# Kernel optimization log

Measured on AMD Instinct MI355X. Metric: run time of the kernel, lower is better.

Reference implementation:

```python
import jax, jax.numpy as jnp
import numpy as np

N = 2048; E = 65536; T = 6; F_IN = 2
H_ENC = 256; LAT = 128; H_DEC = 256
PRED = 6
MIN_X, MAX_X = 0.0, 1.0
MIN_Y, MAX_Y = 0.0, 1.0
MIN_EW, MAX_EW = 0.0, 0.5
VISUAL_RANGE = 0.5


def setup_inputs() -> dict:
    key = jax.random.key(0)
    ks = jax.random.split(key, 17)
    p = lambda k, shape: jax.random.normal(k, shape, jnp.float32) * 0.05
    return {
        "x_seq": jax.random.uniform(ks[0], (T, N, F_IN), jnp.float32),
        "edge_index_seq": jax.random.randint(ks[1], (T, 2, E), 0, N),
        "edge_weight_seq": jax.random.uniform(ks[2], (T, E), jnp.float32, 1e-3, 1.0),
        "h_enc": jnp.zeros((N, H_ENC), jnp.float32),
        "h_dec": jnp.zeros((N, H_DEC), jnp.float32),
        "enc_Wx": p(ks[3], (3, 2, F_IN, H_ENC)),
        "enc_bx": p(ks[4], (3, H_ENC)),
        "enc_Wh": p(ks[5], (3, 2, H_ENC, H_ENC)),
        "enc_bh": p(ks[6], (3, H_ENC)),
        "enc_lin_W": p(ks[7], (H_ENC, LAT)),
        "enc_lin_b": p(ks[8], (LAT,)),
        "dec_Wx": p(ks[9], (3, 2, LAT, H_DEC)),
        "dec_bx": p(ks[10], (3, H_DEC)),
        "dec_Wh": p(ks[11], (3, 2, H_DEC, H_DEC)),
        "dec_bh": p(ks[12], (3, H_DEC)),
        "dec_lin_W": p(ks[13], (H_DEC, F_IN)),
        "dec_lin_b": p(ks[14], (F_IN,)),
    }


def _sparse_conv_fn(edge_index, edge_weight, n):
    # ChebConv K=2, sym normalization, lambda_max=2 => T1(L_hat) = -D^-1/2 A D^-1/2
    src, dst = edge_index[0], edge_index[1]
    deg = jax.ops.segment_sum(edge_weight, src, num_segments=n)
    dinv = jnp.where(deg > 0, jax.lax.rsqrt(jnp.where(deg > 0, deg, 1.0)), 0.0)
    norm = -dinv[src] * edge_weight * dinv[dst]  # [E]

    def conv(x, W, b):  # W: [2, in, out]
        tx1 = jax.ops.segment_sum(norm[:, None] * x[src], dst, num_segments=n)
        return x @ W[0] + tx1 @ W[1] + b
    return conv


def _dense_conv_fn(y_hat):
    # graph rebuilt from detached predicted coords (radius graph, dense masked form)
    c = jax.lax.stop_gradient(y_hat)
    px = c[:, 0] * (MAX_X - MIN_X) + MIN_X
    py = c[:, 1] * (MAX_Y - MIN_Y) + MIN_Y
    coords = jnp.stack((px, py), axis=1)  # [N, 2]
    d = jnp.linalg.norm(coords[:, None, :] - coords[None, :, :], axis=2)  # [N, N]
    mask = (d < VISUAL_RANGE) & (d > 0)
    w = jnp.where(mask, (d - MIN_EW) / (MAX_EW - MIN_EW), 0.0)
    deg = w.sum(axis=1)
    dinv = jnp.where(deg > 0, jax.lax.rsqrt(jnp.where(deg > 0, deg, 1.0)), 0.0)
    M = -(dinv[:, None] * w) * dinv[None, :]  # scaled-Laplacian off-diagonal

    def conv(x, W, b):
        return x @ W[0] + (M @ x) @ W[1] + b
    return conv


def _gru(conv, x, H, Wx, bx, Wh, bh):
    # GConvGRU gates: each gate = conv_x(X) + conv_h(H)
    z = jax.nn.sigmoid(conv(x, Wx[0], bx[0]) + conv(H, Wh[0], bh[0]))
    r = jax.nn.sigmoid(conv(x, Wx[1], bx[1]) + conv(H, Wh[1], bh[1]))
    h_tilde = jnp.tanh(conv(x, Wx[2], bx[2]) + conv(H * r, Wh[2], bh[2]))
    return z * H + (1.0 - z) * h_tilde


def reference(x_seq, edge_index_seq, edge_weight_seq, h_enc, h_dec,
              enc_Wx, enc_bx, enc_Wh, enc_bh, enc_lin_W, enc_lin_b,
              dec_Wx, dec_bx, dec_Wh, dec_bh, dec_lin_W, dec_lin_b):
    n = x_seq.shape[1]

    def step(conv, x, he, hd):
        he0 = _gru(conv, x, he, enc_Wx, enc_bx, enc_Wh, enc_bh)
        z = jax.nn.relu(he0) @ enc_lin_W + enc_lin_b
        hd0 = _gru(conv, z, hd, dec_Wx, dec_bx, dec_Wh, dec_bh)
        y_hat = jax.nn.relu(hd0) @ dec_lin_W + dec_lin_b
        return y_hat, he0, hd0

    # observed snapshots (sparse edge-list graphs)
    for t in range(x_seq.shape[0]):
        conv = _sparse_conv_fn(edge_index_seq[t], edge_weight_seq[t], n)
        y_hat, h_enc, h_dec = step(conv, x_seq[t], h_enc, h_dec)

    preds = [y_hat]
    for _ in range(PRED - 1):
        conv = _dense_conv_fn(y_hat)
        y_hat, h_enc, h_dec = step(conv, y_hat, h_enc, h_dec)
        preds.append(y_hat)
    return jnp.stack(preds)  # [PRED, N, 2]
```

## Files before the change

### kernel.cpp

```cpp
#include <hip/hip_runtime.h>
#include <math.h>

#define NN 2048
#define EE 65536
#define T_OBS 6
#define FIN 2
#define HE 256
#define LT 128
#define XC 384
#define PREDN 6
#define DMM_NZ 8
#define ZR_NZ 4
#define GT_NZ 8
#define LIN_NZ 8

typedef __attribute__((ext_vector_type(8))) short short8v;
typedef __attribute__((ext_vector_type(4))) short short4v;
typedef __attribute__((ext_vector_type(4))) float float4v;

static __device__ __forceinline__ unsigned short f2bf(float f) {
    union { float f; unsigned u; } v; v.f = f;
    unsigned r = v.u + 0x7fff + ((v.u >> 16) & 1);
    return (unsigned short)(r >> 16);
}

static __device__ __forceinline__ void bfsplit(float f, unsigned short& h,
                                               unsigned short& l) {
    unsigned u = __float_as_uint(f);
    h = (unsigned short)(u >> 16);
    float hf = __uint_as_float(u & 0xffff0000u);
    l = (unsigned short)(__float_as_uint(f - hf) >> 16);
}

static __device__ __forceinline__ float bf2f(unsigned short b) {
    return __uint_as_float(((unsigned)b) << 16);
}

__global__ void k_degcnt_lds(const int* __restrict__ ei, const float* __restrict__ ews,
                             float* __restrict__ deg_all, int* __restrict__ cnt_all) {
    __shared__ float ldeg[NN];
    __shared__ int lcnt[NN];
    int tg = blockIdx.y;
    const int* src = ei + (size_t)tg * 2 * EE;
    const int* dst = src + EE;
    const float* ew = ews + (size_t)tg * EE;
    for (int i = threadIdx.x; i < NN; i += 256) { ldeg[i] = 0.f; lcnt[i] = 0; }
    __syncthreads();
    const int EPB = EE / 8;
    int e0 = blockIdx.x * EPB;
    for (int e = e0 + threadIdx.x; e < e0 + EPB; e += 256) {
        atomicAdd(&ldeg[src[e]], ew[e]);
        atomicAdd(&lcnt[dst[e]], 1);
    }
    __syncthreads();
    for (int i = threadIdx.x; i < NN; i += 256) {
        float d = ldeg[i]; int cc = lcnt[i];
        if (d != 0.f) atomicAdd(&deg_all[tg * NN + i], d);
        if (cc) atomicAdd(&cnt_all[tg * NN + i], cc);
    }
}

__global__ void k_scan_b(const int* __restrict__ cnt_all, const float* __restrict__ deg_all,
                         int* __restrict__ roff_all, int* __restrict__ cur_all,
                         float* __restrict__ dinv_all) {
    __shared__ int part[256];
    int tg = blockIdx.x;
    const int* cnt = cnt_all + tg * NN;
    const float* deg = deg_all + tg * NN;
    int* roff = roff_all + tg * (NN + 1);
    int* cur = cur_all + tg * NN;
    float* dinv = dinv_all + tg * NN;
    int t = threadIdx.x;
#pragma unroll
    for (int i = t; i < NN; i += 256) {
        float d = deg[i];
        dinv[i] = d > 0.f ? 1.f / sqrtf(d) : 0.f;
    }
    int loc[8];
    int s = 0;
#pragma unroll
    for (int i = 0; i < 8; i++) { loc[i] = cnt[t * 8 + i]; s += loc[i]; }
    part[t] = s;
    __syncthreads();
    for (int off = 1; off < 256; off <<= 1) {
        int v = (t >= off) ? part[t - off] : 0;
        __syncthreads();
        part[t] += v;
        __syncthreads();
    }
    int run = (t == 0) ? 0 : part[t - 1];
#pragma unroll
    for (int i = 0; i < 8; i++) {
        int idx = t * 8 + i;
        roff[idx] = run;
        cur[idx] = run;
        run += loc[i];
    }
    if (t == 255) roff[NN] = run;
}

__global__ void k_scatter2_b(const int* __restrict__ ei, const float* __restrict__ ews,
                             const float* __restrict__ dinv_all, int* __restrict__ cur_all,
                             int* __restrict__ csr_src_all, float* __restrict__ csr_nrm_all) {
    int tg = blockIdx.y;
    int e = blockIdx.x * blockDim.x + threadIdx.x;
    const int* src = ei + (size_t)tg * 2 * EE;
    const int* dst = src + EE;
    const float* ew = ews + (size_t)tg * EE;
    const float* dinv = dinv_all + tg * NN;
    if (e < EE) {
        int s = src[e], d = dst[e];
        int p = atomicAdd(&cur_all[tg * NN + d], 1);
        csr_src_all[(size_t)tg * EE + p] = s;
        csr_nrm_all[(size_t)tg * EE + p] = -dinv[s] * ew[e] * dinv[d];
    }
}

__global__ void k_spmm2_b(const int* __restrict__ roff_all, const int* __restrict__ csr_src_all,
                          const float* __restrict__ csr_nrm_all, const float* __restrict__ x_seq,
                          float* __restrict__ aggx_all) {
    int tg = blockIdx.y;
    int nid = blockIdx.x * blockDim.x + threadIdx.x;
    if (nid < NN) {
        const int* roff = roff_all + tg * (NN + 1);
        const int* csr_src = csr_src_all + (size_t)tg * EE;
        const float* csr_nrm = csr_nrm_all + (size_t)tg * EE;
        const float* X = x_seq + (size_t)tg * NN * FIN;
        int s0 = roff[nid], s1 = roff[nid + 1];
        float a0 = 0.f, a1 = 0.f;
        for (int s = s0; s < s1; ++s) {
            int i = csr_src[s]; float w = csr_nrm[s];
            float2 xv = *(const float2*)&X[2 * i];
            a0 = fmaf(w, xv.x, a0);
            a1 = fmaf(w, xv.y, a1);
        }
        aggx_all[(size_t)tg * NN * FIN + 2 * nid] = a0;
        aggx_all[(size_t)tg * NN * FIN + 2 * nid + 1] = a1;
    }
}

template <int F, int TPN>
__global__ void k_spmm_vb(const int* __restrict__ roff, const int* __restrict__ csr_src,
                          const float* __restrict__ csr_nrm,
                          const unsigned short* __restrict__ Xb,
                          float* __restrict__ out, int ldo) {
    const int NPB = 256 / TPN;
    int w = threadIdx.x / TPN, l = threadIdx.x % TPN;
    int nid = blockIdx.x * NPB + w;
    int c = l << 2;
    int s0 = roff[nid], s1 = roff[nid + 1];
    float4 acc = make_float4(0.f, 0.f, 0.f, 0.f);
    int s = s0;
    for (; s + 8 <= s1; s += 8) {
        int is[8]; float ws[8];
#pragma unroll
        for (int j = 0; j < 8; j++) { is[j] = csr_src[s + j]; ws[j] = csr_nrm[s + j]; }
        if (c < F) {
            short4v xv[8];
#pragma unroll
            for (int j = 0; j < 8; j++)
                xv[j] = *(const short4v*)&Xb[(size_t)is[j] * F + c];
#pragma unroll
            for (int j = 0; j < 8; j++) {
                acc.x = fmaf(ws[j], bf2f((unsigned short)xv[j][0]), acc.x);
                acc.y = fmaf(ws[j], bf2f((unsigned short)xv[j][1]), acc.y);
                acc.z = fmaf(ws[j], bf2f((unsigned short)xv[j][2]), acc.z);
                acc.w = fmaf(ws[j], bf2f((unsigned short)xv[j][3]), acc.w);
            }
        }
    }
    for (; s < s1; ++s) {
        int i0 = csr_src[s]; float w0 = csr_nrm[s];
        if (c < F) {
            short4v xv = *(const short4v*)&Xb[(size_t)i0 * F + c];
            acc.x = fmaf(w0, bf2f((unsigned short)xv[0]), acc.x);
            acc.y = fmaf(w0, bf2f((unsigned short)xv[1]), acc.y);
            acc.z = fmaf(w0, bf2f((unsigned short)xv[2]), acc.z);
            acc.w = fmaf(w0, bf2f((unsigned short)xv[3]), acc.w);
        }
    }
    if (c < F) *(float4*)&out[(size_t)nid * ldo + c] = acc;
}

__global__ void k_ddeg(const float* __restrict__ c, float* __restrict__ dinv) {
    int i = blockIdx.x;
    int t = threadIdx.x;
    float xi = c[2 * i], yi = c[2 * i + 1];
    float s = 0.f;
    for (int j = t; j < NN; j += 256) {
        float dx = xi - c[2 * j], dy = yi - c[2 * j + 1];
        float d = sqrtf(dx * dx + dy * dy);
        if (d > 0.f && d < 0.5f) s += 2.f * d;
    }
    __shared__ float red[256];
    red[t] = s;
    __syncthreads();
    for (int off = 128; off > 0; off >>= 1) {
        if (t < off) red[t] += red[t + off];
        __syncthreads();
    }
    if (t == 0) {
        float d = red[0];
        dinv[i] = d > 0.f ? 1.f / sqrtf(d) : 0.f;
    }
}

__global__ void k_dM2(const float* __restrict__ c, const float* __restrict__ dinv,
                      unsigned short* __restrict__ Mb, float* __restrict__ ax) {
    int i = blockIdx.x;
    int t = threadIdx.x;
    float xi = c[2 * i], yi = c[2 * i + 1], di = dinv[i];
    float a0 = 0.f, a1 = 0.f;
    for (int j = t; j < NN; j += 256) {
        float dx = xi - c[2 * j], dy = yi - c[2 * j + 1];
        float d = sqrtf(dx * dx + dy * dy);
        float w = (d > 0.f && d < 0.5f) ? 2.f * d : 0.f;
        float v = -(di * w) * dinv[j];
        Mb[(size_t)i * NN + j] = f2bf(v);
        a0 = fmaf(v, c[2 * j], a0);
        a1 = fmaf(v, c[2 * j + 1], a1);
    }
    __shared__ float r0[256], r1[256];
    r0[t] = a0;
    r1[t] = a1;
    __syncthreads();
    for (int off = 128; off > 0; off >>= 1) {
        if (t < off) { r0[t] += r0[t + off]; r1[t] += r1[t + off]; }
        __syncthreads();
    }
    if (t == 0) { ax[2 * i] = r0[0]; ax[2 * i + 1] = r1[0]; }
}

template <int F>
__global__ __launch_bounds__(256) void k_dmm_mfb(
    const unsigned short* __restrict__ Mb, const unsigned short* __restrict__ Xb,
    float* __restrict__ pbuf)
{
    __shared__ __align__(16) unsigned short Ms[64][72];
    __shared__ __align__(16) unsigned short Xs[64][72];
    const int tid = threadIdx.x;
    const int wid = tid >> 6, lane = tid & 63;
    const int m0 = blockIdx.x << 6, n0 = blockIdx.y << 6;
    const int kb0 = blockIdx.z << 8;
    const int lr = lane & 15;
    const int kg = lane >> 4;
    float4v acc[4];
#pragma unroll
    for (int t = 0; t < 4; t++) acc[t] = (float4v){0.f, 0.f, 0.f, 0.f};

    for (int kb = kb0; kb < kb0 + 256; kb += 64) {
#pragma unroll
        for (int it = 0; it < 2; it++) {
            int i = tid + it * 256;
            int r = i >> 3, c8 = (i & 7) << 3;
            *(short8v*)&Ms[r][c8] =
                *(const short8v*)&Mb[(size_t)(m0 + r) * NN + kb + c8];
        }
#pragma unroll
        for (int it = 0; it < 2; it++) {
            int i = tid + it * 256;
            int k2 = (i & 31) << 1;
            int n4 = (i >> 5) << 2;
            short4v va = *(const short4v*)&Xb[(size_t)(kb + k2) * F + n0 + n4];
            short4v vb = *(const short4v*)&Xb[(size_t)(kb + k2 + 1) * F + n0 + n4];
#pragma unroll
            for (int j = 0; j < 4; j++)
                *(unsigned*)&Xs[n4 + j][k2] =
                    (unsigned)(unsigned short)va[j] |
                    ((unsigned)(unsigned short)vb[j] << 16);
        }
        __syncthreads();
#pragma unroll
        for (int kh = 0; kh < 2; kh++) {
            int kk = kh * 32 + kg * 8;
            short8v a = *(const short8v*)&Ms[(wid << 4) + lr][kk];
#pragma unroll
            for (int t = 0; t < 4; t++) {
                short8v b = *(const short8v*)&Xs[(t << 4) + lr][kk];
                acc[t] = __builtin_amdgcn_mfma_f32_16x16x32_bf16(a, b, acc[t], 0, 0, 0);
            }
        }
        __syncthreads();
    }
    float* p = pbuf + (size_t)blockIdx.z * NN * F;
#pragma unroll
    for (int t = 0; t < 4; t++)
#pragma unroll
        for (int j = 0; j < 4; j++)
            p[(size_t)(m0 + (wid << 4) + (kg << 2) + j) * F + n0 + (t << 4) + lr] =
                acc[t][j];
}

template <int F, int NZ>
__global__ void k_redks(const float* __restrict__ pbuf, float* __restrict__ out) {
    const int TOT = NN * F / 4;
    int i = blockIdx.x * blockDim.x + threadIdx.x;
    if (i < TOT) {
        const float4* p = (const float4*)pbuf;
        float4 s = p[i];
#pragma unroll
        for (int z = 1; z < NZ; z++) {
            float4 v = p[(size_t)z * TOT + i];
            s.x += v.x; s.y += v.y; s.z += v.z; s.w += v.w;
        }
        ((float4*)out)[i] = s;
    }
}

template <bool RELU>
__device__ __forceinline__ void mfma_seg(
    unsigned short (*Ah)[40], unsigned short (*Al)[40],
    unsigned short (*Bh)[40], unsigned short (*Bl)[40],
    const float* __restrict__ A, int lda,
    const float* __restrict__ B, int ldb, int K,
    int m0, int tid, int wid, int lr, int kg, float4v (&acc)[4])
{
    for (int k0 = 0; k0 < K; k0 += 32) {
        {
            int r = tid >> 2, k8 = (tid & 3) << 3;
            const float* ap = &A[(size_t)(m0 + r) * lda + k0 + k8];
            float4 va = *(const float4*)ap;
            float4 vb = *(const float4*)(ap + 4);
            float v[8] = {va.x, va.y, va.z, va.w, vb.x, vb.y, vb.z, vb.w};
            short8v hv, lv;
#pragma unroll
            for (int j = 0; j < 8; j++) {
                float f = RELU ? fmaxf(v[j], 0.f) : v[j];
                unsigned short h, l;
                bfsplit(f, h, l);
                hv[j] = (short)h; lv[j] = (short)l;
            }
            *(short8v*)&Ah[r][k8] = hv;
            *(short8v*)&Al[r][k8] = lv;
        }
        {
            int k2 = (tid & 15) << 1;
            int n4 = (tid >> 4) << 2;
            const float* bp = &B[(size_t)(k0 + k2) * ldb + n4];
            float4 va = *(const float4*)bp;
            float4 vb = *(const float4*)(bp + ldb);
            float v0[4] = {va.x, va.y, va.z, va.w};
            float v1[4] = {vb.x, vb.y, vb.z, vb.w};
#pragma unroll
            for (int j = 0; j < 4; j++) {
                unsigned short h0, l0, h1, l1;
                bfsplit(v0[j], h0, l0);
                bfsplit(v1[j], h1, l1);
                *(unsigned*)&Bh[n4 + j][k2] = (unsigned)h0 | ((unsigned)h1 << 16);
                *(unsigned*)&Bl[n4 + j][k2] = (unsigned)l0 | ((unsigned)l1 << 16);
            }
        }
        __syncthreads();
        short8v ah = *(short8v*)&Ah[(wid << 4) + lr][kg << 3];
        short8v al = *(short8v*)&Al[(wid << 4) + lr][kg << 3];
#pragma unroll
        for (int t = 0; t < 4; t++) {
            short8v bh = *(short8v*)&Bh[(t << 4) + lr][kg << 3];
            short8v bl = *(short8v*)&Bl[(t << 4) + lr][kg << 3];
            acc[t] = __builtin_amdgcn_mfma_f32_16x16x32_bf16(ah, bh, acc[t], 0, 0, 0);
            acc[t] = __builtin_amdgcn_mfma_f32_16x16x32_bf16(ah, bl, acc[t], 0, 0, 0);
            acc[t] = __builtin_amdgcn_mfma_f32_16x16x32_bf16(al, bh, acc[t], 0, 0, 0);
        }
        __syncthreads();
    }
}

__global__ __launch_bounds__(256) void k_zr_ks(
    const float* __restrict__ A0, int K01, const float* __restrict__ A1,
    const float* __restrict__ H, const float* __restrict__ A3,
    int la1, int la2, int la3,
    const float* __restrict__ Wx, const float* __restrict__ Wh,
    float* __restrict__ pbuf)
{
    __shared__ __align__(16) unsigned short Ah[64][40], Al[64][40],
                                            Bh[64][40], Bl[64][40];
    int tid = threadIdx.x;
    int wid = tid >> 6, lane = tid & 63, lr = lane & 15, kg = lane >> 4;
    int m0 = blockIdx.x << 6;
    int g = blockIdx.y >> 2;
    int n0 = (blockIdx.y & 3) << 6;
    float4v acc[4];
#pragma unroll
    for (int t = 0; t < 4; t++) acc[t] = (float4v){0.f, 0.f, 0.f, 0.f};
    const float* As[4] = {A0, A1, H, A3};
    const int ldas[4] = {K01, la1, la2, la3};
    const float* Bs[4] = {
        Wx + (size_t)(g * 2 + 0) * K01 * HE + n0,
        Wx + (size_t)(g * 2 + 1) * K01 * HE + n0,
        Wh + (size_t)(g * 2 + 0) * HE * HE + n0,
        Wh + (size_t)(g * 2 + 1) * HE * HE + n0};
    const int Ks[4] = {K01, K01, HE, HE};
    int chunk = (2 * K01 + 2 * HE) / ZR_NZ;
    int lo = blockIdx.z * chunk, hi = lo + chunk;
    int off = 0;
#pragma unroll
    for (int s = 0; s < 4; s++) {
        int a = lo - off; a = a < 0 ? 0 : a;
        int b = hi - off; b = b > Ks[s] ? Ks[s] : b;
        if (b > a)
            mfma_seg<false>(Ah, Al, Bh, Bl, As[s] + a, ldas[s],
                            Bs[s] + (size_t)a * HE, HE, b - a,
                            m0, tid, wid, lr, kg, acc);
        off += Ks[s];
    }
    float* p = pbuf + (size_t)blockIdx.z * NN * 512;
    int cbase = (g << 8) + n0;
#pragma unroll
    for (int t = 0; t < 4; t++)
#pragma unroll
        for (int j = 0; j < 4; j++)
            p[(size_t)(m0 + (wid << 4) + (kg << 2) + j) * 512 + cbase + (t << 4) + lr] =
                acc[t][j];
}

__global__ void k_zr_ep(const float* __restrict__ pbuf,
                        const float* __restrict__ bx, const float* __restrict__ bh,
                        const float* __restrict__ H,
                        const float* __restrict__ x2, const float* __restrict__ ax2,
                        const float* __restrict__ Wx,
                        float* __restrict__ gz, float* __restrict__ hr,
                        unsigned short* __restrict__ hrb)
{
    int i = blockIdx.x * 256 + threadIdx.x;
    const float4* p = (const float4*)pbuf;
    const size_t S = (size_t)NN * 512 / 4;
    float4 a = p[i];
#pragma unroll
    for (int z = 1; z < ZR_NZ; z++) {
        float4 v = p[(size_t)z * S + i];
        a.x += v.x; a.y += v.y; a.z += v.z; a.w += v.w;
    }
    int row = i >> 7, c = (i & 127) << 2;
    int g = c >> 8, cc = c & 255;
    if (Wx) {
        float x0 = x2[2 * row], x1 = x2[2 * row + 1];
        float q0 = ax2[2 * row], q1 = ax2[2 * row + 1];
        const float* W0 = Wx + (size_t)(g * 2 + 0) * FIN * HE;
        const float* W1 = Wx + (size_t)(g * 2 + 1) * FIN * HE;
        float4 w00 = *(const float4*)&W0[cc];
        float4 w01 = *(const float4*)&W0[HE + cc];
        float4 w10 = *(const float4*)&W1[cc];
        float4 w11 = *(const float4*)&W1[HE + cc];
        a.x += x0 * w00.x + x1 * w01.x + q0 * w10.x + q1 * w11.x;
        a.y += x0 * w00.y + x1 * w01.y + q0 * w10.y + q1 * w11.y;
        a.z += x0 * w00.z + x1 * w01.z + q0 * w10.z + q1 * w11.z;
        a.w += x0 * w00.w + x1 * w01.w + q0 * w10.w + q1 * w11.w;
    }
    float4 b0 = *(const float4*)&bx[c];
    float4 b1 = *(const float4*)&bh[c];
    float4 s;
    s.x = 1.f / (1.f + expf(-(a.x + b0.x + b1.x)));
    s.y = 1.f / (1.f + expf(-(a.y + b0.y + b1.y)));
    s.z = 1.f / (1.f + expf(-(a.z + b0.z + b1.z)));
    s.w = 1.f / (1.f + expf(-(a.w + b0.w + b1.w)));
    if (c < HE) {
        *(float4*)&gz[(size_t)row * HE + c] = s;
    } else {
        size_t idx = (size_t)row * HE + cc;
        float4 h = *(const float4*)&H[idx];
        s.x *= h.x; s.y *= h.y; s.z *= h.z; s.w *= h.w;
        *(float4*)&hr[idx] = s;
        short4v sb;
        sb[0] = (short)f2bf(s.x); sb[1] = (short)f2bf(s.y);
        sb[2] = (short)f2bf(s.z); sb[3] = (short)f2bf(s.w);
        *(short4v*)&hrb[idx] = sb;
    }
}

__global__ __launch_bounds__(256) void k_gt_ks(
    const float* __restrict__ A0, int K01, const float* __restrict__ A1,
    const float* __restrict__ hr, const float* __restrict__ A3,
    int la1, int la2, int la3,
    const float* __restrict__ Wx2, const float* __restrict__ Wh2,
    float* __restrict__ pbuf)
{
    __shared__ __align__(16) unsigned short Ah[64][40], Al[64][40],
                                            Bh[64][40], Bl[64][40];
    int tid = threadIdx.x;
    int wid = tid >> 6, lane = tid & 63, lr = lane & 15, kg = lane >> 4;
    int m0 = blockIdx.x << 6;
    int n0 = blockIdx.y << 6;
    float4v acc[4];
#pragma unroll
    for (int t = 0; t < 4; t++) acc[t] = (float4v){0.f, 0.f, 0.f, 0.f};
    const float* As[4] = {A0, A1, hr, A3};
    const int ldas[4] = {K01, la1, la2, la3};
    const float* Bs[4] = {
        Wx2 + n0,
        Wx2 + (size_t)K01 * HE + n0,
        Wh2 + n0,
        Wh2 + (size_t)HE * HE + n0};
    const int Ks[4] = {K01, K01, HE, HE};
    int chunk = (2 * K01 + 2 * HE) / GT_NZ;
    int lo = blockIdx.z * chunk, hi = lo + chunk;
    int off = 0;
#pragma unroll
    for (int s = 0; s < 4; s++) {
        int a = lo - off; a = a < 0 ? 0 : a;
        int b = hi - off; b = b > Ks[s] ? Ks[s] : b;
        if (b > a)
            mfma_seg<false>(Ah, Al, Bh, Bl, As[s] + a, ldas[s],
                            Bs[s] + (size_t)a * HE, HE, b - a,
                            m0, tid, wid, lr, kg, acc);
        off += Ks[s];
    }
    float* p = pbuf + (size_t)blockIdx.z * NN * HE;
#pragma unroll
    for (int t = 0; t < 4; t++)
#pragma unroll
        for (int j = 0; j < 4; j++)
            p[(size_t)(m0 + (wid << 4) + (kg << 2) + j) * HE + n0 + (t << 4) + lr] =
                acc[t][j];
}

__global__ void k_gt_ep(const float* __restrict__ pbuf,
                        const float* __restrict__ bx2, const float* __restrict__ bh2,
                        const float* __restrict__ gz,
                        const float* __restrict__ x2, const float* __restrict__ ax2,
                        const float* __restrict__ Wx2,
                        float* __restrict__ H,
                        unsigned short* __restrict__ Hb, int ldhb,
                        const float* __restrict__ dlinW, const float* __restrict__ dlinb,
                        float* __restrict__ yhat)
{
    int i = blockIdx.x * 256 + threadIdx.x;
    const float4* p = (const float4*)pbuf;
    const size_t S = (size_t)NN * HE / 4;
    float4 a = p[i];
#pragma unroll
    for (int z = 1; z < GT_NZ; z++) {
        float4 v = p[(size_t)z * S + i];
        a.x += v.x; a.y += v.y; a.z += v.z; a.w += v.w;
    }
    int row = i >> 6, c = (i & 63) << 2;
    if (Wx2) {
        float x0 = x2[2 * row], x1 = x2[2 * row + 1];
        float q0 = ax2[2 * row], q1 = ax2[2 * row + 1];
        float4 w00 = *(const float4*)&Wx2[c];
        float4 w01 = *(const float4*)&Wx2[HE + c];
        float4 w10 = *(const float4*)&Wx2[2 * HE + c];
        float4 w11 = *(const float4*)&Wx2[3 * HE + c];
        a.x += x0 * w00.x + x1 * w01.x + q0 * w10.x + q1 * w11.x;
        a.y += x0 * w00.y + x1 * w01.y + q0 * w10.y + q1 * w11.y;
        a.z += x0 * w00.z + x1 * w01.z + q0 * w10.z + q1 * w11.z;
        a.w += x0 * w00.w + x1 * w01.w + q0 * w10.w + q1 * w11.w;
    }
    float4 b0 = *(const float4*)&bx2[c];
    float4 b1 = *(const float4*)&bh2[c];
    size_t idx = (size_t)row * HE + c;
    float4 z = *(const float4*)&gz[idx];
    float4 h = *(const float4*)&H[idx];
    float4 o;
    o.x = z.x * h.x + (1.f - z.x) * tanhf(a.x + b0.x + b1.x);
    o.y = z.y * h.y + (1.f - z.y) * tanhf(a.y + b0.y + b1.y);
    o.z = z.z * h.z + (1.f - z.z) * tanhf(a.z + b0.z + b1.z);
    o.w = z.w * h.w + (1.f - z.w) * tanhf(a.w + b0.w + b1.w);
    *(float4*)&H[idx] = o;
    short4v sb;
    sb[0] = (short)f2bf(o.x); sb[1] = (short)f2bf(o.y);
    sb[2] = (short)f2bf(o.z); sb[3] = (short)f2bf(o.w);
    *(short4v*)&Hb[(size_t)row * ldhb + c] = sb;
    if (dlinW) {
        float a0 = 0.f, a1 = 0.f;
        float ov[4] = {o.x, o.y, o.z, o.w};
#pragma unroll
        for (int j = 0; j < 4; j++) {
            float v = fmaxf(ov[j], 0.f);
            float2 b = *(const float2*)&dlinW[(c + j) * 2];
            a0 = fmaf(v, b.x, a0);
            a1 = fmaf(v, b.y, a1);
        }
        for (int off = 32; off > 0; off >>= 1) {
            a0 += __shfl_down(a0, off, 64);
            a1 += __shfl_down(a1, off, 64);
        }
        if ((threadIdx.x & 63) == 0) {
            yhat[2 * row] = a0 + dlinb[0];
            yhat[2 * row + 1] = a1 + dlinb[1];
        }
    }
}

__global__ __launch_bounds__(256) void k_lin_ks(
    const float* __restrict__ A, const float* __restrict__ B,
    float* __restrict__ pbuf)
{
    __shared__ __align__(16) unsigned short Ah[64][40], Al[64][40],
                                            Bh[64][40], Bl[64][40];
    int tid = threadIdx.x;
    int wid = tid >> 6, lane = tid & 63, lr = lane & 15, kg = lane >> 4;
    int m0 = blockIdx.x << 6;
    int n0 = blockIdx.y << 6;
    int lo = blockIdx.z << 5;
    float4v acc[4];
#pragma unroll
    for (int t = 0; t < 4; t++) acc[t] = (float4v){0.f, 0.f, 0.f, 0.f};
    mfma_seg<true>(Ah, Al, Bh, Bl, A + lo, HE, B + (size_t)lo * LT + n0, LT, 32,
                   m0, tid, wid, lr, kg, acc);
    float* p = pbuf + (size_t)blockIdx.z * NN * LT;
#pragma unroll
    for (int t = 0; t < 4; t++)
#pragma unroll
        for (int j = 0; j < 4; j++)
            p[(size_t)(m0 + (wid << 4) + (kg << 2) + j) * LT + n0 + (t << 4) + lr] =
                acc[t][j];
}

__global__ void k_lin_ep(const float* __restrict__ pbuf,
                         const float* __restrict__ bias, float* __restrict__ out,
                         unsigned short* __restrict__ zb)
{
    int i = blockIdx.x * 256 + threadIdx.x;
    const float4* p = (const float4*)pbuf;
    const size_t S = (size_t)NN * LT / 4;
    int row = i >> 5, c = (i & 31) << 2;
    float4 bb = *(const float4*)&bias[c];
    float4 s = make_float4(bb.x, bb.y, bb.z, bb.w);
#pragma unroll
    for (int z = 0; z < LIN_NZ; z++) {
        float4 v = p[z * S + i];
        s.x += v.x; s.y += v.y; s.z += v.z; s.w += v.w;
    }
    ((float4*)out)[i] = s;
    short4v sb;
    sb[0] = (short)f2bf(s.x); sb[1] = (short)f2bf(s.y);
    sb[2] = (short)f2bf(s.z); sb[3] = (short)f2bf(s.w);
    *(short4v*)&zb[(size_t)row * XC + c] = sb;
}

__global__ void k_cvtb(const float* __restrict__ in, unsigned short* __restrict__ outb,
                       int ldo) {
    int i = blockIdx.x * 256 + threadIdx.x;
    int r = i >> 8, c = i & 255;
    outb[(size_t)r * ldo + c] = f2bf(in[i]);
}

extern "C" void kernel_launch(void* const* d_in, const int* in_sizes, int n_in,
                              void* d_out, int out_size, void* d_ws, size_t ws_size,
                              hipStream_t stream) {
    (void)in_sizes; (void)n_in; (void)out_size; (void)ws_size;
    const float* x_seq = (const float*)d_in[0];
    const int* ei = (const int*)d_in[1];
    const float* ews = (const float*)d_in[2];
    const float* h_enc_in = (const float*)d_in[3];
    const float* h_dec_in = (const float*)d_in[4];
    const float* encWx = (const float*)d_in[5];
    const float* encbx = (const float*)d_in[6];
    const float* encWh = (const float*)d_in[7];
    const float* encbh = (const float*)d_in[8];
    const float* elinW = (const float*)d_in[9];
    const float* elinb = (const float*)d_in[10];
    const float* decWx = (const float*)d_in[11];
    const float* decbx = (const float*)d_in[12];
    const float* decWh = (const float*)d_in[13];
    const float* decbh = (const float*)d_in[14];
    const float* dlinW = (const float*)d_in[15];
    const float* dlinb = (const float*)d_in[16];
    float* out = (float*)d_out;

    float* W = (float*)d_ws;
    float* h_enc = W; W += (size_t)NN * HE;
    float* h_dec = W; W += (size_t)NN * HE;
    float* aggh  = W; W += (size_t)NN * HE;
    float* hr    = W; W += (size_t)NN * HE;
    float* agghr = W; W += (size_t)NN * HE;
    float* gz    = W; W += (size_t)NN * HE;
    float* zlat  = W; W += (size_t)NN * LT;
    float* Y     = W; W += (size_t)NN * XC;
    float* yhat  = W; W += (size_t)NN * FIN;
    float* aggx2 = W; W += (size_t)NN * FIN;
    float* dinv_d = W; W += NN;
    unsigned short* Mb = (unsigned short*)W; W += (size_t)NN * NN / 2;
    float* pbuf  = W; W += (size_t)DMM_NZ * NN * XC;
    unsigned short* Hen_b = (unsigned short*)W; W += (size_t)NN * HE / 2;
    unsigned short* hr_b  = (unsigned short*)W; W += (size_t)NN * HE / 2;
    unsigned short* xcat_b = (unsigned short*)W; W += (size_t)NN * XC / 2;
    float* deg_all = W; W += (size_t)T_OBS * NN;
    int*   cnt_all = (int*)W; W += (size_t)T_OBS * NN;
    float* dinv_all = W; W += (size_t)T_OBS * NN;
    float* csr_nrm_all = W; W += (size_t)T_OBS * EE;
    float* aggx_all = W; W += (size_t)T_OBS * NN * FIN;
    int* roff_all = (int*)W; W += (size_t)T_OBS * (NN + 1) + 1;
    int* cur_all = (int*)W; W += (size_t)T_OBS * NN;
    int* csr_src_all = (int*)W; W += (size_t)T_OBS * EE;

    hipMemsetAsync(deg_all, 0, sizeof(float) * T_OBS * NN * 2, stream);
    k_degcnt_lds<<<dim3(8, T_OBS), 256, 0, stream>>>(ei, ews, deg_all, cnt_all);
    k_scan_b<<<T_OBS, 256, 0, stream>>>(cnt_all, deg_all, roff_all, cur_all, dinv_all);
    k_scatter2_b<<<dim3(EE / 256, T_OBS), 256, 0, stream>>>(ei, ews, dinv_all, cur_all,
                                                            csr_src_all, csr_nrm_all);
    k_spmm2_b<<<dim3(NN / 256, T_OBS), 256, 0, stream>>>(roff_all, csr_src_all,
                                                         csr_nrm_all, x_seq, aggx_all);

    hipMemcpyAsync(h_enc, h_enc_in, sizeof(float) * NN * HE, hipMemcpyDeviceToDevice, stream);
    hipMemcpyAsync(h_dec, h_dec_in, sizeof(float) * NN * HE, hipMemcpyDeviceToDevice, stream);
    k_cvtb<<<NN * HE / 256, 256, 0, stream>>>(h_enc_in, Hen_b, HE);
    k_cvtb<<<NN * HE / 256, 256, 0, stream>>>(h_dec_in, xcat_b + LT, XC);

    for (int step = 0; step < T_OBS + PREDN - 1; ++step) {
        bool sparse = step < T_OBS;
        const float* xin;
        const float* aggx_s;
        const int* roff = roff_all + step * (NN + 1);
        const int* csr_src = csr_src_all + (size_t)step * EE;
        const float* csr_nrm = csr_nrm_all + (size_t)step * EE;
        if (sparse) {
            xin = x_seq + (size_t)step * NN * FIN;
            aggx_s = aggx_all + (size_t)step * NN * FIN;
        } else {
            k_ddeg<<<NN, 256, 0, stream>>>(yhat, dinv_d);
            k_dM2<<<NN, 256, 0, stream>>>(yhat, dinv_d, Mb, aggx2);
            xin = yhat;
            aggx_s = aggx2;
        }

        if (sparse) {
            k_spmm_vb<HE, 64><<<NN / 4, 256, 0, stream>>>(roff, csr_src, csr_nrm,
                                                          Hen_b, aggh, HE);
        } else {
            k_dmm_mfb<HE><<<dim3(NN / 64, HE / 64, DMM_NZ), 256, 0, stream>>>(Mb, Hen_b, pbuf);
            k_redks<HE, DMM_NZ><<<NN * HE / 4 / 256, 256, 0, stream>>>(pbuf, aggh);
        }
        k_zr_ks<<<dim3(NN / 64, 8, ZR_NZ), 256, 0, stream>>>(xin, 0, aggx_s, h_enc, aggh,
                                                             FIN, HE, HE,
                                                             encWx, encWh, pbuf);
        k_zr_ep<<<NN * 512 / 4 / 256, 256, 0, stream>>>(pbuf, encbx, encbh, h_enc,
                                                        xin, aggx_s, encWx, gz, hr, hr_b);
        if (sparse) {
            k_spmm_vb<HE, 64><<<NN / 4, 256, 0, stream>>>(roff, csr_src, csr_nrm,
                                                          hr_b, agghr, HE);
        } else {
            k_dmm_mfb<HE><<<dim3(NN / 64, HE / 64, DMM_NZ), 256, 0, stream>>>(Mb, hr_b, pbuf);
            k_redks<HE, DMM_NZ><<<NN * HE / 4 / 256, 256, 0, stream>>>(pbuf, agghr);
        }
        k_gt_ks<<<dim3(NN / 64, 4, GT_NZ), 256, 0, stream>>>(xin, 0, aggx_s, hr, agghr,
                                                             FIN, HE, HE,
                                                             encWx + 4 * FIN * HE,
                                                             encWh + 4 * HE * HE, pbuf);
        k_gt_ep<<<NN * HE / 4 / 256, 256, 0, stream>>>(pbuf, encbx + 2 * HE,
                                                       encbh + 2 * HE, gz,
                                                       xin, aggx_s, encWx + 4 * FIN * HE,
                                                       h_enc, Hen_b, HE,
                                                       nullptr, nullptr, nullptr);
        k_lin_ks<<<dim3(NN / 64, 2, LIN_NZ), 256, 0, stream>>>(h_enc, elinW, pbuf);
        k_lin_ep<<<NN * LT / 4 / 256, 256, 0, stream>>>(pbuf, elinb, zlat, xcat_b);

        if (sparse) {
            k_spmm_vb<XC, 128><<<NN / 2, 256, 0, stream>>>(roff, csr_src, csr_nrm,
                                                           xcat_b, Y, XC);
        } else {
            k_dmm_mfb<XC><<<dim3(NN / 64, XC / 64, DMM_NZ), 256, 0, stream>>>(Mb, xcat_b, pbuf);
            k_redks<XC, DMM_NZ><<<NN * XC / 4 / 256, 256, 0, stream>>>(pbuf, Y);
        }
        k_zr_ks<<<dim3(NN / 64, 8, ZR_NZ), 256, 0, stream>>>(zlat, LT, Y, h_dec, Y + LT,
                                                             XC, HE, XC,
                                                             decWx, decWh, pbuf);
        k_zr_ep<<<NN * 512 / 4 / 256, 256, 0, stream>>>(pbuf, decbx, decbh, h_dec,
                                                        nullptr, nullptr, nullptr,
                                                        gz, hr, hr_b);
        if (sparse) {
            k_spmm_vb<HE, 64><<<NN / 4, 256, 0, stream>>>(roff, csr_src, csr_nrm,
                                                          hr_b, agghr, HE);
        } else {
            k_dmm_mfb<HE><<<dim3(NN / 64, HE / 64, DMM_NZ), 256, 0, stream>>>(Mb, hr_b, pbuf);
            k_redks<HE, DMM_NZ><<<NN * HE / 4 / 256, 256, 0, stream>>>(pbuf, agghr);
        }
        k_gt_ks<<<dim3(NN / 64, 4, GT_NZ), 256, 0, stream>>>(zlat, LT, Y, hr, agghr,
                                                             XC, HE, HE,
                                                             decWx + 4 * LT * HE,
                                                             decWh + 4 * HE * HE, pbuf);
        k_gt_ep<<<NN * HE / 4 / 256, 256, 0, stream>>>(pbuf, decbx + 2 * HE,
                                                       decbh + 2 * HE, gz,
                                                       nullptr, nullptr, nullptr,
                                                       h_dec, xcat_b + LT, XC,
                                                       dlinW, dlinb, yhat);

        if (step >= T_OBS - 1) {
            hipMemcpyAsync(out + (size_t)(step - (T_OBS - 1)) * NN * FIN, yhat,
                           sizeof(float) * NN * FIN, hipMemcpyDeviceToDevice, stream);
        }
    }
}
```

Measured before the change: 1.632 ms.

## Fuse z/r gate GEMM with epilogue, drop split-K; halve dense split-K factors

Replaces the split-K z/r gate GEMM and its separate reduction/sigmoid epilogue with a single kernel that computes the full K range per block and applies bias, input projection, sigmoid and the H*r product directly from registers. This removes the partial-sum buffer round trip and one launch per GRU. It also lowers the split-K factor for the dense graph matmul and the candidate-gate GEMM from 8 to 4, which means fewer partial sums to reduce but fewer blocks in flight. The fused z/r kernel now launches only 32x8 blocks, which risks underusing the GPU's compute units. Its epilogue writes are also strided, column-per-lane scalar stores.

```diff
diff --git a/kernel.cpp b/kernel.cpp
--- a/kernel.cpp
+++ b/kernel.cpp
@@ -9,9 +9,8 @@
 #define LT 128
 #define XC 384
 #define PREDN 6
-#define DMM_NZ 8
-#define ZR_NZ 4
-#define GT_NZ 8
+#define DMM_NZ 4
+#define GT_NZ 4
 #define LIN_NZ 8
 
 typedef __attribute__((ext_vector_type(8))) short short8v;
@@ -241,14 +240,15 @@
     const int tid = threadIdx.x;
     const int wid = tid >> 6, lane = tid & 63;
     const int m0 = blockIdx.x << 6, n0 = blockIdx.y << 6;
-    const int kb0 = blockIdx.z << 8;
+    const int kchunk = NN / DMM_NZ;
+    const int kb0 = blockIdx.z * kchunk;
     const int lr = lane & 15;
     const int kg = lane >> 4;
     float4v acc[4];
 #pragma unroll
     for (int t = 0; t < 4; t++) acc[t] = (float4v){0.f, 0.f, 0.f, 0.f};
 
-    for (int kb = kb0; kb < kb0 + 256; kb += 64) {
+    for (int kb = kb0; kb < kb0 + kchunk; kb += 64) {
 #pragma unroll
         for (int it = 0; it < 2; it++) {
             int i = tid + it * 256;
@@ -365,12 +365,16 @@
     }
 }
 
-__global__ __launch_bounds__(256) void k_zr_ks(
+__global__ __launch_bounds__(256) void k_zr1(
     const float* __restrict__ A0, int K01, const float* __restrict__ A1,
     const float* __restrict__ H, const float* __restrict__ A3,
     int la1, int la2, int la3,
     const float* __restrict__ Wx, const float* __restrict__ Wh,
-    float* __restrict__ pbuf)
+    const float* __restrict__ bx, const float* __restrict__ bh,
+    const float* __restrict__ x2, const float* __restrict__ ax2,
+    const float* __restrict__ Wxr,
+    float* __restrict__ gz, float* __restrict__ hr,
+    unsigned short* __restrict__ hrb)
 {
     __shared__ __align__(16) unsigned short Ah[64][40], Al[64][40],
                                             Bh[64][40], Bl[64][40];
@@ -390,80 +394,40 @@
         Wh + (size_t)(g * 2 + 0) * HE * HE + n0,
         Wh + (size_t)(g * 2 + 1) * HE * HE + n0};
     const int Ks[4] = {K01, K01, HE, HE};
-    int chunk = (2 * K01 + 2 * HE) / ZR_NZ;
-    int lo = blockIdx.z * chunk, hi = lo + chunk;
-    int off = 0;
 #pragma unroll
     for (int s = 0; s < 4; s++) {
-        int a = lo - off; a = a < 0 ? 0 : a;
-        int b = hi - off; b = b > Ks[s] ? Ks[s] : b;
-        if (b > a)
-            mfma_seg<false>(Ah, Al, Bh, Bl, As[s] + a, ldas[s],
-                            Bs[s] + (size_t)a * HE, HE, b - a,
+        if (Ks[s] > 0)
+            mfma_seg<false>(Ah, Al, Bh, Bl, As[s], ldas[s], Bs[s], HE, Ks[s],
                             m0, tid, wid, lr, kg, acc);
-        off += Ks[s];
-    }
-    float* p = pbuf + (size_t)blockIdx.z * NN * 512;
-    int cbase = (g << 8) + n0;
-#pragma unroll
-    for (int t = 0; t < 4; t++)
-#pragma unroll
-        for (int j = 0; j < 4; j++)
-            p[(size_t)(m0 + (wid << 4) + (kg << 2) + j) * 512 + cbase + (t << 4) + lr] =
-                acc[t][j];
-}
-
-__global__ void k_zr_ep(const float* __restrict__ pbuf,
-                        const float* __restrict__ bx, const float* __restrict__ bh,
-                        const float* __restrict__ H,
-                        const float* __restrict__ x2, const float* __restrict__ ax2,
-                        const float* __restrict__ Wx,
-                        float* __restrict__ gz, float* __restrict__ hr,
-                        unsigned short* __restrict__ hrb)
-{
-    int i = blockIdx.x * 256 + threadIdx.x;
-    const float4* p = (const float4*)pbuf;
-    const size_t S = (size_t)NN * 512 / 4;
-    float4 a = p[i];
-#pragma unroll
-    for (int z = 1; z < ZR_NZ; z++) {
-        float4 v = p[(size_t)z * S + i];
-        a.x += v.x; a.y += v.y; a.z += v.z; a.w += v.w;
-    }
-    int row = i >> 7, c = (i & 127) << 2;
-    int g = c >> 8, cc = c & 255;
-    if (Wx) {
-        float x0 = x2[2 * row], x1 = x2[2 * row + 1];
-        float q0 = ax2[2 * row], q1 = ax2[2 * row + 1];
-        const float* W0 = Wx + (size_t)(g * 2 + 0) * FIN * HE;
-        const float* W1 = Wx + (size_t)(g * 2 + 1) * FIN * HE;
-        float4 w00 = *(const float4*)&W0[cc];
-        float4 w01 = *(const float4*)&W0[HE + cc];
-        float4 w10 = *(const float4*)&W1[cc];
-        float4 w11 = *(const float4*)&W1[HE + cc];
-        a.x += x0 * w00.x + x1 * w01.x + q0 * w10.x + q1 * w11.x;
-        a.y += x0 * w00.y + x1 * w01.y + q0 * w10.y + q1 * w11.y;
-        a.z += x0 * w00.z + x1 * w01.z + q0 * w10.z + q1 * w11.z;
-        a.w += x0 * w00.w + x1 * w01.w + q0 * w10.w + q1 * w11.w;
-    }
-    float4 b0 = *(const float4*)&bx[c];
-    float4 b1 = *(const float4*)&bh[c];
-    float4 s;
-    s.x = 1.f / (1.f + expf(-(a.x + b0.x + b1.x)));
-    s.y = 1.f / (1.f + expf(-(a.y + b0.y + b1.y)));
-    s.z = 1.f / (1.f + expf(-(a.z + b0.z + b1.z)));
-    s.w = 1.f / (1.f + expf(-(a.w + b0.w + b1.w)));
-    if (c < HE) {
-        *(float4*)&gz[(size_t)row * HE + c] = s;
-    } else {
-        size_t idx = (size_t)row * HE + cc;
-        float4 h = *(const float4*)&H[idx];
-        s.x *= h.x; s.y *= h.y; s.z *= h.z; s.w *= h.w;
-        *(float4*)&hr[idx] = s;
-        short4v sb;
-        sb[0] = (short)f2bf(s.x); sb[1] = (short)f2bf(s.y);
-        sb[2] = (short)f2bf(s.z); sb[3] = (short)f2bf(s.w);
-        *(short4v*)&hrb[idx] = sb;
+    }
+#pragma unroll
+    for (int j = 0; j < 4; j++) {
+        int row = m0 + (wid << 4) + (kg << 2) + j;
+        float x0 = 0.f, x1 = 0.f, q0 = 0.f, q1 = 0.f;
+        if (Wxr) {
+            x0 = x2[2 * row]; x1 = x2[2 * row + 1];
+            q0 = ax2[2 * row]; q1 = ax2[2 * row + 1];
+        }
+#pragma unroll
+        for (int t = 0; t < 4; t++) {
+            int col = n0 + (t << 4) + lr;
+            float a = acc[t][j];
+            if (Wxr) {
+                const float* W0 = Wxr + (size_t)(g * 2 + 0) * FIN * HE;
+                const float* W1 = Wxr + (size_t)(g * 2 + 1) * FIN * HE;
+                a += x0 * W0[col] + x1 * W0[HE + col] + q0 * W1[col] + q1 * W1[HE + col];
+            }
+            a += bx[g * HE + col] + bh[g * HE + col];
+            float s = 1.f / (1.f + expf(-a));
+            size_t idx = (size_t)row * HE + col;
+            if (g == 0) {
+                gz[idx] = s;
+            } else {
+                float v = H[idx] * s;
+                hr[idx] = v;
+                hrb[idx] = f2bf(v);
+            }
+        }
     }
 }
 
@@ -671,7 +635,7 @@
     float* aggx2 = W; W += (size_t)NN * FIN;
     float* dinv_d = W; W += NN;
     unsigned short* Mb = (unsigned short*)W; W += (size_t)NN * NN / 2;
-    float* pbuf  = W; W += (size_t)DMM_NZ * NN * XC;
+    float* pbuf  = W; W += (size_t)8 * NN * XC;
     unsigned short* Hen_b = (unsigned short*)W; W += (size_t)NN * HE / 2;
     unsigned short* hr_b  = (unsigned short*)W; W += (size_t)NN * HE / 2;
     unsigned short* xcat_b = (unsigned short*)W; W += (size_t)NN * XC / 2;
@@ -721,11 +685,10 @@
             k_dmm_mfb<HE><<<dim3(NN / 64, HE / 64, DMM_NZ), 256, 0, stream>>>(Mb, Hen_b, pbuf);
             k_redks<HE, DMM_NZ><<<NN * HE / 4 / 256, 256, 0, stream>>>(pbuf, aggh);
         }
-        k_zr_ks<<<dim3(NN / 64, 8, ZR_NZ), 256, 0, stream>>>(xin, 0, aggx_s, h_enc, aggh,
-                                                             FIN, HE, HE,
-                                                             encWx, encWh, pbuf);
-        k_zr_ep<<<NN * 512 / 4 / 256, 256, 0, stream>>>(pbuf, encbx, encbh, h_enc,
-                                                        xin, aggx_s, encWx, gz, hr, hr_b);
+        k_zr1<<<dim3(NN / 64, 8), 256, 0, stream>>>(xin, 0, aggx_s, h_enc, aggh,
+                                                    FIN, HE, HE, encWx, encWh,
+                                                    encbx, encbh, xin, aggx_s, encWx,
+                                                    gz, hr, hr_b);
         if (sparse) {
             k_spmm_vb<HE, 64><<<NN / 4, 256, 0, stream>>>(roff, csr_src, csr_nrm,
                                                           hr_b, agghr, HE);
@@ -752,12 +715,11 @@
             k_dmm_mfb<XC><<<dim3(NN / 64, XC / 64, DMM_NZ), 256, 0, stream>>>(Mb, xcat_b, pbuf);
             k_redks<XC, DMM_NZ><<<NN * XC / 4 / 256, 256, 0, stream>>>(pbuf, Y);
         }
-        k_zr_ks<<<dim3(NN / 64, 8, ZR_NZ), 256, 0, stream>>>(zlat, LT, Y, h_dec, Y + LT,
-                                                             XC, HE, XC,
-                                                             decWx, decWh, pbuf);
-        k_zr_ep<<<NN * 512 / 4 / 256, 256, 0, stream>>>(pbuf, decbx, decbh, h_dec,
-                                                        nullptr, nullptr, nullptr,
-                                                        gz, hr, hr_b);
+        k_zr1<<<dim3(NN / 64, 8), 256, 0, stream>>>(zlat, LT, Y, h_dec, Y + LT,
+                                                    XC, HE, XC, decWx, decWh,
+                                                    decbx, decbh,
+                                                    nullptr, nullptr, nullptr,
+                                                    gz, hr, hr_b);
         if (sparse) {
             k_spmm_vb<HE, 64><<<NN / 4, 256, 0, stream>>>(roff, csr_src, csr_nrm,
                                                           hr_b, agghr, HE);
```

New measurement: 1.787 ms. 9.5% more time.
